# Kernel optimization log

Measured on AMD Instinct MI355X. Metric: run time of the kernel, lower is better.

Reference implementation:

```python
import jax, jax.numpy as jnp
import numpy as np
from jax import lax

VOCAB = 50000
EMB = 10
HID = 16


def setup_inputs() -> dict:
    key = jax.random.key(0)
    ks = jax.random.split(key, 8)
    B, T = 4096, 512
    x = jax.random.randint(ks[0], (B, T), 0, VOCAB + 1)
    emb = jax.random.normal(ks[1], (VOCAB + 1, EMB), dtype=jnp.float32)
    emb = emb.at[0].set(0.0)  # padding_idx=0 row is zeros
    s_ih = 1.0 / np.sqrt(HID)
    Wih = jax.random.uniform(ks[2], (4 * HID, EMB), minval=-s_ih, maxval=s_ih, dtype=jnp.float32)
    Whh = jax.random.uniform(ks[3], (4 * HID, HID), minval=-s_ih, maxval=s_ih, dtype=jnp.float32)
    bih = jax.random.uniform(ks[4], (4 * HID,), minval=-s_ih, maxval=s_ih, dtype=jnp.float32)
    bhh = jax.random.uniform(ks[5], (4 * HID,), minval=-s_ih, maxval=s_ih, dtype=jnp.float32)
    Wfc = jax.random.uniform(ks[6], (1, HID), minval=-s_ih, maxval=s_ih, dtype=jnp.float32)
    bfc = jax.random.uniform(ks[7], (1,), minval=-s_ih, maxval=s_ih, dtype=jnp.float32)
    return {"x": x, "emb": emb, "Wih": Wih, "Whh": Whh, "bih": bih, "bhh": bhh, "Wfc": Wfc, "bfc": bfc}


def _lstm_last_h(xe, Wih, Whh, bih, bhh):
    # xe: [B, T, EMB] -> final hidden state [B, HID]. PyTorch gate order: i, f, g, o.
    B = xe.shape[0]
    h0 = jnp.zeros((B, HID), dtype=xe.dtype)
    c0 = jnp.zeros((B, HID), dtype=xe.dtype)
    # Precompute input projections for all timesteps: [T, B, 4H]
    xproj = jnp.einsum('btе,ge->btg'.replace('\u0435', 'e'), xe, Wih) + bih + bhh
    xproj = xproj.transpose(1, 0, 2)

    def step(carry, xp_t):
        h, c = carry
        gates = xp_t + h @ Whh.T  # [B, 4H]
        i, f, g, o = jnp.split(gates, 4, axis=-1)
        i = jax.nn.sigmoid(i)
        f = jax.nn.sigmoid(f)
        g = jnp.tanh(g)
        o = jax.nn.sigmoid(o)
        c = f * c + i * g
        h = o * jnp.tanh(c)
        return (h, c), None

    (h, _), _ = lax.scan(step, (h0, c0), xproj)
    return h


def reference(x, emb, Wih, Whh, bih, bhh, Wfc, bfc):
    xe = emb[x]  # [B, T, EMB] embedding lookup (padding row 0 is zero)
    h = _lstm_last_h(xe, Wih, Whh, bih, bhh)  # [B, HID]
    out = h @ Wfc.T + bfc  # [B, 1]
    return jax.nn.sigmoid(out)
```

## Files before the change

kernel.cpp:

```cpp
#include <hip/hip_runtime.h>

#define T_LEN 512
#define NHID 16
#define NEMB 10
#define VOCAB1 50001

typedef float v2f __attribute__((ext_vector_type(2)));

__global__ __launch_bounds__(256) void build_table(
    const float* __restrict__ emb, const float* __restrict__ Wih,
    const float* __restrict__ bih, const float* __restrict__ bhh,
    float* __restrict__ tbl)
{
    const int tid = blockIdx.x * 256 + threadIdx.x;
    if (tid >= VOCAB1 * 16) return;
    const int v = tid >> 4, j = tid & 15;
    float e[NEMB];
    #pragma unroll
    for (int i = 0; i < NEMB; ++i) e[i] = emb[v * NEMB + i];
    float o[4];
    #pragma unroll
    for (int q = 0; q < 4; ++q) {
        const int r = q * 16 + j;
        float a = bih[r] + bhh[r];
        #pragma unroll
        for (int i = 0; i < NEMB; ++i) a += e[i] * Wih[r * NEMB + i];
        o[q] = a;
    }
    ((float4*)tbl)[tid] = make_float4(o[0], o[1], o[2], o[3]);
}

__global__ __launch_bounds__(256) void lstm_pipe_kernel(
    const int*   __restrict__ x,
    const float* __restrict__ tbl,
    const float* __restrict__ Whh,
    const float* __restrict__ Wfc,
    const float* __restrict__ bfc,
    float*       __restrict__ out)
{
    __shared__ int   idx_lds[T_LEN + 8][17];
    __shared__ float hx[16][20];

    const int tid  = threadIdx.x;
    const int lane = tid & 63;
    const int j    = lane & 15;
    const int lb   = tid >> 4;
    const int batch = blockIdx.x * 16 + lb;

    for (int i = tid; i < 16 * (T_LEN + 8); i += 256) {
        const int b = i & 15;
        const int t = i >> 4;
        idx_lds[t][b] = (t < T_LEN) ? x[(blockIdx.x * 16 + b) * T_LEN + t] : 0;
    }

    v2f w[4][8];
    #pragma unroll
    for (int q = 0; q < 4; ++q) {
        const int r = j + 16 * q;
        #pragma unroll
        for (int p = 0; p < 8; ++p)
            w[q][p] = (v2f){Whh[r * NHID + 2 * p], Whh[r * NHID + 2 * p + 1]};
    }

    __syncthreads();

    v2f h2[8];
    #pragma unroll
    for (int p = 0; p < 8; ++p) h2[p] = (v2f){0.f, 0.f};
    float c = 0.f;

    const float NL2E  = -1.44269504088896f;
    const float NL2E2 = -2.88539008177793f;
    const float4* t4 = (const float4*)tbl;
    const float4* hp = (const float4*)&hx[lb][0];

    float4 pf[4];
    #pragma unroll
    for (int s = 0; s < 4; ++s)
        pf[s] = t4[(long)idx_lds[s][lb] * 16 + j];

    #pragma unroll 1
    for (int t = 0; t < T_LEN; t += 4) {
        #pragma unroll
        for (int u = 0; u < 4; ++u) {
            const float4 tb = pf[u];
            pf[u] = t4[(long)idx_lds[t + 4 + u][lb] * 16 + j];

            v2f a0 = (v2f){tb.x, 0.f}, a1 = (v2f){tb.y, 0.f};
            v2f a2 = (v2f){tb.z, 0.f}, a3 = (v2f){tb.w, 0.f};
            #pragma unroll
            for (int p = 0; p < 8; ++p) {
                a0 += h2[p] * w[0][p];
                a1 += h2[p] * w[1][p];
                a2 += h2[p] * w[2][p];
                a3 += h2[p] * w[3][p];
            }
            const float vi = a0.x + a0.y, vf = a1.x + a1.y;
            const float vg = a2.x + a2.y, vo = a3.x + a3.y;

            const float ig = __builtin_amdgcn_rcpf(1.f + __builtin_amdgcn_exp2f(vi * NL2E));
            const float fg = __builtin_amdgcn_rcpf(1.f + __builtin_amdgcn_exp2f(vf * NL2E));
            const float gg = 2.f * __builtin_amdgcn_rcpf(1.f + __builtin_amdgcn_exp2f(vg * NL2E2)) - 1.f;
            const float og = __builtin_amdgcn_rcpf(1.f + __builtin_amdgcn_exp2f(vo * NL2E));

            c = fg * c + ig * gg;
            const float tc = 2.f * __builtin_amdgcn_rcpf(1.f + __builtin_amdgcn_exp2f(c * NL2E2)) - 1.f;
            const float hv = og * tc;

            hx[lb][j] = hv;
            const float4 b0 = hp[0], b1 = hp[1], b2 = hp[2], b3 = hp[3];
            h2[0] = (v2f){b0.x, b0.y}; h2[1] = (v2f){b0.z, b0.w};
            h2[2] = (v2f){b1.x, b1.y}; h2[3] = (v2f){b1.z, b1.w};
            h2[4] = (v2f){b2.x, b2.y}; h2[5] = (v2f){b2.z, b2.w};
            h2[6] = (v2f){b3.x, b3.y}; h2[7] = (v2f){b3.z, b3.w};
        }
    }

    if (j == 0) {
        float logit = bfc[0];
        #pragma unroll
        for (int p = 0; p < 8; ++p)
            logit += h2[p].x * Wfc[2 * p] + h2[p].y * Wfc[2 * p + 1];
        out[batch] = __builtin_amdgcn_rcpf(1.f + __builtin_amdgcn_exp2f(logit * NL2E));
    }
}

__global__ __launch_bounds__(256) void lstm_fb_kernel(
    const int*   __restrict__ x,
    const float* __restrict__ emb,
    const float* __restrict__ Wih,
    const float* __restrict__ Whh,
    const float* __restrict__ bih,
    const float* __restrict__ bhh,
    const float* __restrict__ Wfc,
    const float* __restrict__ bfc,
    float*       __restrict__ out)
{
    __shared__ int   idx_lds[T_LEN][17];
    __shared__ float hx[16][20];

    const int tid  = threadIdx.x;
    const int lane = tid & 63;
    const int j    = lane & 15;
    const int lb   = tid >> 4;
    const int batch = blockIdx.x * 16 + lb;

    for (int i = tid; i < 16 * T_LEN; i += 256) {
        const int b = i & 15;
        const int t = i >> 4;
        idx_lds[t][b] = x[(blockIdx.x * 16 + b) * T_LEN + t];
    }

    float wih[4][NEMB], bias[4];
    v2f w[4][8];
    #pragma unroll
    for (int q = 0; q < 4; ++q) {
        const int r = j + 16 * q;
        #pragma unroll
        for (int e = 0; e < NEMB; ++e) wih[q][e] = Wih[r * NEMB + e];
        #pragma unroll
        for (int p = 0; p < 8; ++p)
            w[q][p] = (v2f){Whh[r * NHID + 2 * p], Whh[r * NHID + 2 * p + 1]};
        bias[q] = bih[r] + bhh[r];
    }

    __syncthreads();

    v2f h2[8];
    #pragma unroll
    for (int p = 0; p < 8; ++p) h2[p] = (v2f){0.f, 0.f};
    float c = 0.f;

    const float NL2E  = -1.44269504088896f;
    const float NL2E2 = -2.88539008177793f;
    const float4* hp = (const float4*)&hx[lb][0];

    float2 xa, xb, xc, xd, xe2;
    {
        const float2* er = (const float2*)(emb + (long)idx_lds[0][lb] * NEMB);
        xa = er[0]; xb = er[1]; xc = er[2]; xd = er[3]; xe2 = er[4];
    }
    int idx_n = idx_lds[1][lb];

    #pragma unroll 1
    for (int t = 0; t < T_LEN; ++t) {
        const float xv[NEMB] = {xa.x, xa.y, xb.x, xb.y, xc.x, xc.y,
                                xd.x, xd.y, xe2.x, xe2.y};
        if (t + 1 < T_LEN) {
            const float2* er = (const float2*)(emb + (long)idx_n * NEMB);
            xa = er[0]; xb = er[1]; xc = er[2]; xd = er[3]; xe2 = er[4];
        }
        const int idx_nn = (t + 2 < T_LEN) ? idx_lds[t + 2][lb] : 0;

        float v[4];
        #pragma unroll
        for (int q = 0; q < 4; ++q) {
            float a = bias[q];
            #pragma unroll
            for (int e = 0; e < NEMB; ++e) a += xv[e] * wih[q][e];
            v[q] = a;
        }
        v2f a0 = (v2f){v[0], 0.f}, a1 = (v2f){v[1], 0.f};
        v2f a2 = (v2f){v[2], 0.f}, a3 = (v2f){v[3], 0.f};
        #pragma unroll
        for (int p = 0; p < 8; ++p) {
            a0 += h2[p] * w[0][p];
            a1 += h2[p] * w[1][p];
            a2 += h2[p] * w[2][p];
            a3 += h2[p] * w[3][p];
        }
        const float vi = a0.x + a0.y, vf = a1.x + a1.y;
        const float vg = a2.x + a2.y, vo = a3.x + a3.y;

        const float ig = __builtin_amdgcn_rcpf(1.f + __builtin_amdgcn_exp2f(vi * NL2E));
        const float fg = __builtin_amdgcn_rcpf(1.f + __builtin_amdgcn_exp2f(vf * NL2E));
        const float gg = 2.f * __builtin_amdgcn_rcpf(1.f + __builtin_amdgcn_exp2f(vg * NL2E2)) - 1.f;
        const float og = __builtin_amdgcn_rcpf(1.f + __builtin_amdgcn_exp2f(vo * NL2E));

        c = fg * c + ig * gg;
        const float tc = 2.f * __builtin_amdgcn_rcpf(1.f + __builtin_amdgcn_exp2f(c * NL2E2)) - 1.f;
        const float hv = og * tc;

        hx[lb][j] = hv;
        const float4 b0 = hp[0], b1 = hp[1], b2 = hp[2], b3 = hp[3];
        h2[0] = (v2f){b0.x, b0.y}; h2[1] = (v2f){b0.z, b0.w};
        h2[2] = (v2f){b1.x, b1.y}; h2[3] = (v2f){b1.z, b1.w};
        h2[4] = (v2f){b2.x, b2.y}; h2[5] = (v2f){b2.z, b2.w};
        h2[6] = (v2f){b3.x, b3.y}; h2[7] = (v2f){b3.z, b3.w};

        idx_n = idx_nn;
    }

    if (j == 0) {
        float logit = bfc[0];
        #pragma unroll
        for (int p = 0; p < 8; ++p)
            logit += h2[p].x * Wfc[2 * p] + h2[p].y * Wfc[2 * p + 1];
        out[batch] = __builtin_amdgcn_rcpf(1.f + __builtin_amdgcn_exp2f(logit * NL2E));
    }
}

extern "C" void kernel_launch(void* const* d_in, const int* in_sizes, int n_in,
                              void* d_out, int out_size, void* d_ws, size_t ws_size,
                              hipStream_t stream) {
    const int*   x   = (const int*)  d_in[0];
    const float* emb = (const float*)d_in[1];
    const float* Wih = (const float*)d_in[2];
    const float* Whh = (const float*)d_in[3];
    const float* bih = (const float*)d_in[4];
    const float* bhh = (const float*)d_in[5];
    const float* Wfc = (const float*)d_in[6];
    const float* bfc = (const float*)d_in[7];
    float* outp = (float*)d_out;

    const int B = in_sizes[0] / T_LEN;
    const size_t TABLE_BYTES = (size_t)VOCAB1 * 64 * sizeof(float);

    if (ws_size >= TABLE_BYTES) {
        float* tbl = (float*)d_ws;
        build_table<<<(VOCAB1 * 16 + 255) / 256, 256, 0, stream>>>(emb, Wih, bih, bhh, tbl);
        lstm_pipe_kernel<<<B / 16, 256, 0, stream>>>(x, tbl, Whh, Wfc, bfc, outp);
    } else {
        lstm_fb_kernel<<<B / 16, 256, 0, stream>>>(x, emb, Wih, Whh, bih, bhh, Wfc, bfc, outp);
    }
}
```

Before: 155.1 us.

## Compute LSTM recurrent matvec with fp16 MFMA, one wave per 16 sequences

Replaces the per-lane scalar h·Whh dot products and LDS broadcast of h with four 16x16x16 f16 MFMA instructions per step. Each 64-thread block handles 16 batch rows, and the gate accumulators come straight from the prefetched table values. The table layout changes to a plain row-major [vocab][64] so gate columns can be fed as MFMA C operands. This removes the LDS round trip and the many VALU FMAs per step on the serial recurrence. It adds fp16 rounding of h and Whh, which may cost accuracy, and uses 4x fewer threads per block (64 instead of 256).

```diff
diff --git a/kernel.cpp b/kernel.cpp
--- a/kernel.cpp
+++ b/kernel.cpp
@@ -4,33 +4,27 @@
 #define NHID 16
 #define NEMB 10
 #define VOCAB1 50001
+#define ISTR 524
 
 typedef float v2f __attribute__((ext_vector_type(2)));
-
-__global__ __launch_bounds__(256) void build_table(
+typedef float v4f __attribute__((ext_vector_type(4)));
+typedef _Float16 v4h __attribute__((ext_vector_type(4)));
+
+__global__ __launch_bounds__(256) void build_table_r(
     const float* __restrict__ emb, const float* __restrict__ Wih,
     const float* __restrict__ bih, const float* __restrict__ bhh,
     float* __restrict__ tbl)
 {
     const int tid = blockIdx.x * 256 + threadIdx.x;
-    if (tid >= VOCAB1 * 16) return;
-    const int v = tid >> 4, j = tid & 15;
-    float e[NEMB];
-    #pragma unroll
-    for (int i = 0; i < NEMB; ++i) e[i] = emb[v * NEMB + i];
-    float o[4];
-    #pragma unroll
-    for (int q = 0; q < 4; ++q) {
-        const int r = q * 16 + j;
-        float a = bih[r] + bhh[r];
-        #pragma unroll
-        for (int i = 0; i < NEMB; ++i) a += e[i] * Wih[r * NEMB + i];
-        o[q] = a;
-    }
-    ((float4*)tbl)[tid] = make_float4(o[0], o[1], o[2], o[3]);
-}
-
-__global__ __launch_bounds__(256) void lstm_pipe_kernel(
+    if (tid >= VOCAB1 * 64) return;
+    const int v = tid >> 6, r = tid & 63;
+    float a = bih[r] + bhh[r];
+    #pragma unroll
+    for (int e = 0; e < NEMB; ++e) a += emb[v * NEMB + e] * Wih[r * NEMB + e];
+    tbl[tid] = a;
+}
+
+__global__ __launch_bounds__(64) void lstm_mfma_kernel(
     const int*   __restrict__ x,
     const float* __restrict__ tbl,
     const float* __restrict__ Whh,
@@ -38,91 +32,85 @@
     const float* __restrict__ bfc,
     float*       __restrict__ out)
 {
-    __shared__ int   idx_lds[T_LEN + 8][17];
-    __shared__ float hx[16][20];
-
-    const int tid  = threadIdx.x;
-    const int lane = tid & 63;
-    const int j    = lane & 15;
-    const int lb   = tid >> 4;
-    const int batch = blockIdx.x * 16 + lb;
-
-    for (int i = tid; i < 16 * (T_LEN + 8); i += 256) {
-        const int b = i & 15;
-        const int t = i >> 4;
-        idx_lds[t][b] = (t < T_LEN) ? x[(blockIdx.x * 16 + b) * T_LEN + t] : 0;
-    }
-
-    v2f w[4][8];
+    __shared__ int idxs[16 * ISTR];
+
+    const int l = threadIdx.x;
+    const int n = l & 15;
+    const int p = l >> 4;
+    const int base = blockIdx.x * 16;
+
+    #pragma unroll 1
+    for (int b = 0; b < 16; ++b) {
+        const int* xr = x + (long)(base + b) * T_LEN;
+        for (int t = l; t < ISTR; t += 64)
+            idxs[b * ISTR + t] = (t < T_LEN) ? (xr[t] << 4) : 0;
+    }
+    __syncthreads();
+
+    v4h wA[4];
     #pragma unroll
     for (int q = 0; q < 4; ++q) {
-        const int r = j + 16 * q;
-        #pragma unroll
-        for (int p = 0; p < 8; ++p)
-            w[q][p] = (v2f){Whh[r * NHID + 2 * p], Whh[r * NHID + 2 * p + 1]};
-    }
-
-    __syncthreads();
-
-    v2f h2[8];
-    #pragma unroll
-    for (int p = 0; p < 8; ++p) h2[p] = (v2f){0.f, 0.f};
-    float c = 0.f;
+        const int r = q * 16 + n;
+        #pragma unroll
+        for (int j = 0; j < 4; ++j)
+            wA[q][j] = (_Float16)Whh[r * NHID + 4 * p + j];
+    }
+
+    float h[4] = {0.f, 0.f, 0.f, 0.f};
+    float c[4] = {0.f, 0.f, 0.f, 0.f};
 
     const float NL2E  = -1.44269504088896f;
     const float NL2E2 = -2.88539008177793f;
-    const float4* t4 = (const float4*)tbl;
-    const float4* hp = (const float4*)&hx[lb][0];
-
-    float4 pf[4];
-    #pragma unroll
-    for (int s = 0; s < 4; ++s)
-        pf[s] = t4[(long)idx_lds[s][lb] * 16 + j];
+    const v4f* t4 = (const v4f*)tbl;
+    const int* myidx = &idxs[n * ISTR];
+
+    v4f pf[4][4];
+    #pragma unroll
+    for (int s = 0; s < 4; ++s) {
+        const int iv = myidx[s] + p;
+        #pragma unroll
+        for (int q = 0; q < 4; ++q) pf[s][q] = t4[iv + q * 4];
+    }
 
     #pragma unroll 1
     for (int t = 0; t < T_LEN; t += 4) {
         #pragma unroll
         for (int u = 0; u < 4; ++u) {
-            const float4 tb = pf[u];
-            pf[u] = t4[(long)idx_lds[t + 4 + u][lb] * 16 + j];
-
-            v2f a0 = (v2f){tb.x, 0.f}, a1 = (v2f){tb.y, 0.f};
-            v2f a2 = (v2f){tb.z, 0.f}, a3 = (v2f){tb.w, 0.f};
+            v4h hb;
             #pragma unroll
-            for (int p = 0; p < 8; ++p) {
-                a0 += h2[p] * w[0][p];
-                a1 += h2[p] * w[1][p];
-                a2 += h2[p] * w[2][p];
-                a3 += h2[p] * w[3][p];
+            for (int j = 0; j < 4; ++j) hb[j] = (_Float16)h[j];
+
+            const v4f d0 = __builtin_amdgcn_mfma_f32_16x16x16f16(wA[0], hb, pf[u][0], 0, 0, 0);
+            const v4f d1 = __builtin_amdgcn_mfma_f32_16x16x16f16(wA[1], hb, pf[u][1], 0, 0, 0);
+            const v4f d2 = __builtin_amdgcn_mfma_f32_16x16x16f16(wA[2], hb, pf[u][2], 0, 0, 0);
+            const v4f d3 = __builtin_amdgcn_mfma_f32_16x16x16f16(wA[3], hb, pf[u][3], 0, 0, 0);
+
+            {
+                const int iv = myidx[t + 4 + u] + p;
+                #pragma unroll
+                for (int q = 0; q < 4; ++q) pf[u][q] = t4[iv + q * 4];
             }
-            const float vi = a0.x + a0.y, vf = a1.x + a1.y;
-            const float vg = a2.x + a2.y, vo = a3.x + a3.y;
-
-            const float ig = __builtin_amdgcn_rcpf(1.f + __builtin_amdgcn_exp2f(vi * NL2E));
-            const float fg = __builtin_amdgcn_rcpf(1.f + __builtin_amdgcn_exp2f(vf * NL2E));
-            const float gg = 2.f * __builtin_amdgcn_rcpf(1.f + __builtin_amdgcn_exp2f(vg * NL2E2)) - 1.f;
-            const float og = __builtin_amdgcn_rcpf(1.f + __builtin_amdgcn_exp2f(vo * NL2E));
-
-            c = fg * c + ig * gg;
-            const float tc = 2.f * __builtin_amdgcn_rcpf(1.f + __builtin_amdgcn_exp2f(c * NL2E2)) - 1.f;
-            const float hv = og * tc;
-
-            hx[lb][j] = hv;
-            const float4 b0 = hp[0], b1 = hp[1], b2 = hp[2], b3 = hp[3];
-            h2[0] = (v2f){b0.x, b0.y}; h2[1] = (v2f){b0.z, b0.w};
-            h2[2] = (v2f){b1.x, b1.y}; h2[3] = (v2f){b1.z, b1.w};
-            h2[4] = (v2f){b2.x, b2.y}; h2[5] = (v2f){b2.z, b2.w};
-            h2[6] = (v2f){b3.x, b3.y}; h2[7] = (v2f){b3.z, b3.w};
-        }
-    }
-
-    if (j == 0) {
-        float logit = bfc[0];
-        #pragma unroll
-        for (int p = 0; p < 8; ++p)
-            logit += h2[p].x * Wfc[2 * p] + h2[p].y * Wfc[2 * p + 1];
-        out[batch] = __builtin_amdgcn_rcpf(1.f + __builtin_amdgcn_exp2f(logit * NL2E));
-    }
+
+            #pragma unroll
+            for (int j = 0; j < 4; ++j) {
+                const float ig = __builtin_amdgcn_rcpf(1.f + __builtin_amdgcn_exp2f(d0[j] * NL2E));
+                const float fg = __builtin_amdgcn_rcpf(1.f + __builtin_amdgcn_exp2f(d1[j] * NL2E));
+                const float gg = 2.f * __builtin_amdgcn_rcpf(1.f + __builtin_amdgcn_exp2f(d2[j] * NL2E2)) - 1.f;
+                const float og = __builtin_amdgcn_rcpf(1.f + __builtin_amdgcn_exp2f(d3[j] * NL2E));
+                c[j] = fg * c[j] + ig * gg;
+                const float tc = 2.f * __builtin_amdgcn_rcpf(1.f + __builtin_amdgcn_exp2f(c[j] * NL2E2)) - 1.f;
+                h[j] = og * tc;
+            }
+        }
+    }
+
+    float s = 0.f;
+    #pragma unroll
+    for (int j = 0; j < 4; ++j) s += h[j] * Wfc[4 * p + j];
+    s += __shfl_xor(s, 16, 64);
+    s += __shfl_xor(s, 32, 64);
+    if (p == 0)
+        out[base + n] = __builtin_amdgcn_rcpf(1.f + __builtin_amdgcn_exp2f((s + bfc[0]) * NL2E));
 }
 
 __global__ __launch_bounds__(256) void lstm_fb_kernel(
@@ -258,8 +246,8 @@
 
     if (ws_size >= TABLE_BYTES) {
         float* tbl = (float*)d_ws;
-        build_table<<<(VOCAB1 * 16 + 255) / 256, 256, 0, stream>>>(emb, Wih, bih, bhh, tbl);
-        lstm_pipe_kernel<<<B / 16, 256, 0, stream>>>(x, tbl, Whh, Wfc, bfc, outp);
+        build_table_r<<<(VOCAB1 * 64 + 255) / 256, 256, 0, stream>>>(emb, Wih, bih, bhh, tbl);
+        lstm_mfma_kernel<<<B / 16, 64, 0, stream>>>(x, tbl, Whh, Wfc, bfc, outp);
     } else {
         lstm_fb_kernel<<<B / 16, 256, 0, stream>>>(x, emb, Wih, Whh, bih, bhh, Wfc, bfc, outp);
     }
```

Measured after the change: 307.5 us. 98.3% more time.

## Broadcast hidden state via DPP row rotates instead of LDS round-trip

Applied to the files above, without the earlier changes.

Replaces the per-step LDS write/read of the hidden vector with 15 DPP row_ror moves inside each 16-lane row. The recurrent weights are pre-permuted to match the rotated order, so the matvec becomes plain scalar FMAs with no pairwise reduction. The index staging is reorganized with pre-shifted indices in a per-batch-row layout, and the final FC uses a shuffle reduction. This targets the LDS latency on the serial recurrence's critical path, at the cost of more VALU/DPP instructions per step.

```diff
diff --git a/kernel.cpp b/kernel.cpp
--- a/kernel.cpp
+++ b/kernel.cpp
@@ -4,6 +4,7 @@
 #define NHID 16
 #define NEMB 10
 #define VOCAB1 50001
+#define IROW 520
 
 typedef float v2f __attribute__((ext_vector_type(2)));
 
@@ -30,7 +31,11 @@
     ((float4*)tbl)[tid] = make_float4(o[0], o[1], o[2], o[3]);
 }
 
-__global__ __launch_bounds__(256) void lstm_pipe_kernel(
+#define DPP_ROR(dst, src_i, r)                                                   \
+    dst = __builtin_bit_cast(float, __builtin_amdgcn_update_dpp(                 \
+              0, src_i, 0x120 + r, 0xF, 0xF, true))
+
+__global__ __launch_bounds__(256) void lstm_dpp_kernel(
     const int*   __restrict__ x,
     const float* __restrict__ tbl,
     const float* __restrict__ Whh,
@@ -38,91 +43,86 @@
     const float* __restrict__ bfc,
     float*       __restrict__ out)
 {
-    __shared__ int   idx_lds[T_LEN + 8][17];
-    __shared__ float hx[16][20];
-
-    const int tid  = threadIdx.x;
-    const int lane = tid & 63;
-    const int j    = lane & 15;
-    const int lb   = tid >> 4;
+    __shared__ int idxs[16][IROW];
+
+    const int tid = threadIdx.x;
+    const int j   = tid & 15;
+    const int lb  = tid >> 4;
     const int batch = blockIdx.x * 16 + lb;
 
-    for (int i = tid; i < 16 * (T_LEN + 8); i += 256) {
-        const int b = i & 15;
-        const int t = i >> 4;
-        idx_lds[t][b] = (t < T_LEN) ? x[(blockIdx.x * 16 + b) * T_LEN + t] : 0;
-    }
-
-    v2f w[4][8];
+    #pragma unroll 1
+    for (int b = 0; b < 16; ++b) {
+        const int* xr = x + (size_t)(blockIdx.x * 16 + b) * T_LEN;
+        for (int t = tid; t < IROW; t += 256)
+            idxs[b][t] = (t < T_LEN) ? (xr[t] << 4) : 0;
+    }
+    __syncthreads();
+
+    float w[4][16];
     #pragma unroll
     for (int q = 0; q < 4; ++q) {
-        const int r = j + 16 * q;
-        #pragma unroll
-        for (int p = 0; p < 8; ++p)
-            w[q][p] = (v2f){Whh[r * NHID + 2 * p], Whh[r * NHID + 2 * p + 1]};
-    }
-
-    __syncthreads();
-
-    v2f h2[8];
-    #pragma unroll
-    for (int p = 0; p < 8; ++p) h2[p] = (v2f){0.f, 0.f};
-    float c = 0.f;
-
+        const int row = (q * 16 + j) * NHID;
+        #pragma unroll
+        for (int r = 0; r < 16; ++r)
+            w[q][r] = Whh[row + ((j - r) & 15)];
+    }
+
+    float h = 0.f, c = 0.f;
     const float NL2E  = -1.44269504088896f;
     const float NL2E2 = -2.88539008177793f;
     const float4* t4 = (const float4*)tbl;
-    const float4* hp = (const float4*)&hx[lb][0];
 
     float4 pf[4];
     #pragma unroll
     for (int s = 0; s < 4; ++s)
-        pf[s] = t4[(long)idx_lds[s][lb] * 16 + j];
+        pf[s] = t4[idxs[lb][s] + j];
 
     #pragma unroll 1
     for (int t = 0; t < T_LEN; t += 4) {
         #pragma unroll
         for (int u = 0; u < 4; ++u) {
             const float4 tb = pf[u];
-            pf[u] = t4[(long)idx_lds[t + 4 + u][lb] * 16 + j];
-
-            v2f a0 = (v2f){tb.x, 0.f}, a1 = (v2f){tb.y, 0.f};
-            v2f a2 = (v2f){tb.z, 0.f}, a3 = (v2f){tb.w, 0.f};
+            pf[u] = t4[idxs[lb][t + 4 + u] + j];
+
+            float hr[16];
+            const int hvi = __builtin_bit_cast(int, h);
+            hr[0] = h;
+            DPP_ROR(hr[1],  hvi, 1);   DPP_ROR(hr[2],  hvi, 2);
+            DPP_ROR(hr[3],  hvi, 3);   DPP_ROR(hr[4],  hvi, 4);
+            DPP_ROR(hr[5],  hvi, 5);   DPP_ROR(hr[6],  hvi, 6);
+            DPP_ROR(hr[7],  hvi, 7);   DPP_ROR(hr[8],  hvi, 8);
+            DPP_ROR(hr[9],  hvi, 9);   DPP_ROR(hr[10], hvi, 10);
+            DPP_ROR(hr[11], hvi, 11);  DPP_ROR(hr[12], hvi, 12);
+            DPP_ROR(hr[13], hvi, 13);  DPP_ROR(hr[14], hvi, 14);
+            DPP_ROR(hr[15], hvi, 15);
+
+            float a0 = tb.x, a1 = tb.y, a2 = tb.z, a3 = tb.w;
             #pragma unroll
-            for (int p = 0; p < 8; ++p) {
-                a0 += h2[p] * w[0][p];
-                a1 += h2[p] * w[1][p];
-                a2 += h2[p] * w[2][p];
-                a3 += h2[p] * w[3][p];
+            for (int r = 0; r < 16; ++r) {
+                a0 = fmaf(hr[r], w[0][r], a0);
+                a1 = fmaf(hr[r], w[1][r], a1);
+                a2 = fmaf(hr[r], w[2][r], a2);
+                a3 = fmaf(hr[r], w[3][r], a3);
             }
-            const float vi = a0.x + a0.y, vf = a1.x + a1.y;
-            const float vg = a2.x + a2.y, vo = a3.x + a3.y;
-
-            const float ig = __builtin_amdgcn_rcpf(1.f + __builtin_amdgcn_exp2f(vi * NL2E));
-            const float fg = __builtin_amdgcn_rcpf(1.f + __builtin_amdgcn_exp2f(vf * NL2E));
-            const float gg = 2.f * __builtin_amdgcn_rcpf(1.f + __builtin_amdgcn_exp2f(vg * NL2E2)) - 1.f;
-            const float og = __builtin_amdgcn_rcpf(1.f + __builtin_amdgcn_exp2f(vo * NL2E));
+
+            const float ig = __builtin_amdgcn_rcpf(1.f + __builtin_amdgcn_exp2f(a0 * NL2E));
+            const float fg = __builtin_amdgcn_rcpf(1.f + __builtin_amdgcn_exp2f(a1 * NL2E));
+            const float gg = 2.f * __builtin_amdgcn_rcpf(1.f + __builtin_amdgcn_exp2f(a2 * NL2E2)) - 1.f;
+            const float og = __builtin_amdgcn_rcpf(1.f + __builtin_amdgcn_exp2f(a3 * NL2E));
 
             c = fg * c + ig * gg;
             const float tc = 2.f * __builtin_amdgcn_rcpf(1.f + __builtin_amdgcn_exp2f(c * NL2E2)) - 1.f;
-            const float hv = og * tc;
-
-            hx[lb][j] = hv;
-            const float4 b0 = hp[0], b1 = hp[1], b2 = hp[2], b3 = hp[3];
-            h2[0] = (v2f){b0.x, b0.y}; h2[1] = (v2f){b0.z, b0.w};
-            h2[2] = (v2f){b1.x, b1.y}; h2[3] = (v2f){b1.z, b1.w};
-            h2[4] = (v2f){b2.x, b2.y}; h2[5] = (v2f){b2.z, b2.w};
-            h2[6] = (v2f){b3.x, b3.y}; h2[7] = (v2f){b3.z, b3.w};
-        }
-    }
-
-    if (j == 0) {
-        float logit = bfc[0];
-        #pragma unroll
-        for (int p = 0; p < 8; ++p)
-            logit += h2[p].x * Wfc[2 * p] + h2[p].y * Wfc[2 * p + 1];
-        out[batch] = __builtin_amdgcn_rcpf(1.f + __builtin_amdgcn_exp2f(logit * NL2E));
-    }
+            h = og * tc;
+        }
+    }
+
+    float s = h * Wfc[j];
+    s += __shfl_xor(s, 1, 64);
+    s += __shfl_xor(s, 2, 64);
+    s += __shfl_xor(s, 4, 64);
+    s += __shfl_xor(s, 8, 64);
+    if (j == 0)
+        out[batch] = __builtin_amdgcn_rcpf(1.f + __builtin_amdgcn_exp2f((s + bfc[0]) * NL2E));
 }
 
 __global__ __launch_bounds__(256) void lstm_fb_kernel(
@@ -259,7 +259,7 @@
     if (ws_size >= TABLE_BYTES) {
         float* tbl = (float*)d_ws;
         build_table<<<(VOCAB1 * 16 + 255) / 256, 256, 0, stream>>>(emb, Wih, bih, bhh, tbl);
-        lstm_pipe_kernel<<<B / 16, 256, 0, stream>>>(x, tbl, Whh, Wfc, bfc, outp);
+        lstm_dpp_kernel<<<B / 16, 256, 0, stream>>>(x, tbl, Whh, Wfc, bfc, outp);
     } else {
         lstm_fb_kernel<<<B / 16, 256, 0, stream>>>(x, emb, Wih, Whh, bih, bhh, Wfc, bfc, outp);
     }
```

After: 180.1 us. 1.16x slower.
